# Optimization experiments

Hardware: AMD Instinct MI355X
Metric: run time of the kernel (lower is better)

The kernel has to match this reference:

```python
import jax, jax.numpy as jnp
import numpy as np

B, L, QD, KVD, H = 8, 1024, 1024, 768, 16
DH = QD // H
EPS = 1e-5


def setup_inputs() -> dict:
    key = jax.random.key(0)
    ks = jax.random.split(key, 12)
    q = jax.random.normal(ks[0], (B, L, QD), jnp.float32)
    k = jax.random.normal(ks[1], (B, L, KVD), jnp.float32)
    v = jax.random.normal(ks[2], (B, L, KVD), jnp.float32)
    # key_padding_mask: True = valid token (code masks where ~mask)
    lengths = jax.random.randint(ks[3], (B,), L // 2, L + 1)
    key_padding_mask = jnp.arange(L)[None, :] < lengths[:, None]
    def lin(kk, fan_in, fan_out):
        bound = 1.0 / np.sqrt(fan_in)
        k1, k2 = jax.random.split(kk)
        W = jax.random.uniform(k1, (fan_out, fan_in), jnp.float32, -bound, bound)
        b = jax.random.uniform(k2, (fan_out,), jnp.float32, -bound, bound)
        return W, b
    Wq, bq = lin(ks[4], QD, QD)
    Wk, bk = lin(ks[5], KVD, QD)
    Wv, bv = lin(ks[6], KVD, QD)
    Wo, bo = lin(ks[7], QD, QD)
    gamma = jnp.ones((QD,), jnp.float32)
    beta = jnp.zeros((QD,), jnp.float32)
    return {"q": q, "k": k, "v": v, "key_padding_mask": key_padding_mask,
            "Wq": Wq, "bq": bq, "Wk": Wk, "bk": bk, "Wv": Wv, "bv": bv,
            "Wo": Wo, "bo": bo, "gamma": gamma, "beta": beta}


def reference(q, k, v, key_padding_mask, Wq, bq, Wk, bk, Wv, bv, Wo, bo, gamma, beta):
    Bq, Lq, C = q.shape
    scale = DH ** -0.5
    # projections -> [B, H, L, DH]
    qh = (q @ Wq.T + bq).reshape(Bq, Lq, H, DH).transpose(0, 2, 1, 3)
    kh = (k @ Wk.T + bk).reshape(Bq, Lq, H, DH).transpose(0, 2, 1, 3)
    vh = (v @ Wv.T + bv).reshape(Bq, Lq, H, DH).transpose(0, 2, 1, 3)
    attn = jnp.einsum('bhld,bhmd->bhlm', qh, kh) * scale
    attn = jnp.where(key_padding_mask[:, None, None, :], attn, -jnp.inf)
    p = jax.nn.softmax(attn, axis=-1)
    out = jnp.einsum('bhlm,bhmd->bhld', p, vh).transpose(0, 2, 1, 3).reshape(Bq, Lq, C)
    out = out @ Wo.T + bo  # dropout is identity in eval
    y = out + q
    mu = jnp.mean(y, axis=-1, keepdims=True)
    var = jnp.var(y, axis=-1, keepdims=True)
    return (y - mu) * jax.lax.rsqrt(var + EPS) * gamma + beta
```

## Files before the change

kernel.cpp:

```cpp
#include <hip/hip_runtime.h>
#include <stdint.h>

typedef float f32x4 __attribute__((ext_vector_type(4)));
typedef __bf16 bf16x8 __attribute__((ext_vector_type(8)));
typedef unsigned short u16;

__device__ __forceinline__ void gload_lds16(const void* g, void* l) {
  __builtin_amdgcn_global_load_lds(
      (__attribute__((address_space(1))) void*)(uintptr_t)(g),
      (__attribute__((address_space(3))) void*)(uint32_t)(uintptr_t)(l),
      16, 0, 0);
}

__device__ __forceinline__ u16 f2bf(float x) {
  __bf16 h = (__bf16)x;
  return *(u16*)&h;
}

__global__ __launch_bounds__(256) void cast_all(
    const float* __restrict__ q, const float* __restrict__ k,
    const float* __restrict__ v, const float* __restrict__ wq,
    const float* __restrict__ wk, const float* __restrict__ wv,
    const float* __restrict__ wo, u16* __restrict__ out) {
  const int g = blockIdx.x;
  const float* in;
  int s;
  if (g < 8192) { in = q; s = 0; }
  else if (g < 14336) { in = k; s = 8192; }
  else if (g < 20480) { in = v; s = 14336; }
  else if (g < 21504) { in = wq; s = 20480; }
  else if (g < 22272) { in = wk; s = 21504; }
  else if (g < 23040) { in = wv; s = 22272; }
  else { in = wo; s = 23040; }
  const int li = (g - s) * 256 + threadIdx.x;
  float4 x = *((const float4*)in + li);
  unsigned lo = (unsigned)f2bf(x.x) | ((unsigned)f2bf(x.y) << 16);
  unsigned hi = (unsigned)f2bf(x.z) | ((unsigned)f2bf(x.w) << 16);
  ((uint2*)out)[(size_t)g * 256 + threadIdx.x] = make_uint2(lo, hi);
}

__global__ __launch_bounds__(256) void proj_kernel(
    const u16* __restrict__ qb, const u16* __restrict__ kb,
    const u16* __restrict__ vb, const u16* __restrict__ wqb,
    const u16* __restrict__ wkb, const u16* __restrict__ wvb,
    const float* __restrict__ bq, const float* __restrict__ bk,
    const float* __restrict__ bv, u16* __restrict__ qpb,
    u16* __restrict__ kpb, u16* __restrict__ vtb) {
  __shared__ __align__(16) u16 As[128 * 32];
  __shared__ __align__(16) u16 Bs[128 * 32];
  const int tid = threadIdx.x;
  const int role = blockIdx.y >> 3;
  const int m0 = blockIdx.x * 128, n0 = (blockIdx.y & 7) * 128;
  const int K = (role == 0) ? 1024 : 768;
  const u16* A = (role == 0) ? qb : ((role == 1) ? kb : vb);
  const u16* Bt = (role == 0) ? wqb : ((role == 1) ? wkb : wvb);
  const float* bias = (role == 0) ? bq : ((role == 1) ? bk : bv);
  const int lane = tid & 63, w = tid >> 6;
  const int wr = w >> 1, wc = w & 1;
  const int l16 = lane & 15, lk = lane >> 4;
  const int srow = tid >> 2, schunk = tid & 3;

  const u16* Ap = A + (size_t)(m0 + srow) * K + schunk * 8;
  const u16* Bp = Bt + (size_t)(n0 + srow) * K + schunk * 8;

  f32x4 acc[4][4] = {};

  for (int kt = 0; kt < K; kt += 32) {
#pragma unroll
    for (int p = 0; p < 2; ++p) {
      gload_lds16(Ap + (size_t)p * 64 * K + kt, As + tid * 8 + p * 2048);
      gload_lds16(Bp + (size_t)p * 64 * K + kt, Bs + tid * 8 + p * 2048);
    }
    __syncthreads();
    bf16x8 a[4], b[4];
#pragma unroll
    for (int i = 0; i < 4; ++i)
      a[i] = *(const bf16x8*)(As + (wr * 64 + i * 16 + l16) * 32 + lk * 8);
#pragma unroll
    for (int j = 0; j < 4; ++j)
      b[j] = *(const bf16x8*)(Bs + (wc * 64 + j * 16 + l16) * 32 + lk * 8);
#pragma unroll
    for (int i = 0; i < 4; ++i)
#pragma unroll
      for (int j = 0; j < 4; ++j)
        acc[i][j] = __builtin_amdgcn_mfma_f32_16x16x32_bf16(a[i], b[j], acc[i][j], 0, 0, 0);
    __syncthreads();
  }

#pragma unroll
  for (int i = 0; i < 4; ++i) {
    const int mrow = m0 + wr * 64 + i * 16 + lk * 4;
#pragma unroll
    for (int j = 0; j < 4; ++j) {
      const int col = n0 + wc * 64 + j * 16 + l16;
      const float bval = bias[col];
      if (role == 0) {
#pragma unroll
        for (int r = 0; r < 4; ++r)
          qpb[(size_t)(mrow + r) * 1024 + col] = f2bf(acc[i][j][r] + bval);
      } else if (role == 1) {
#pragma unroll
        for (int r = 0; r < 4; ++r)
          kpb[(size_t)(mrow + r) * 1024 + col] = f2bf(acc[i][j][r] + bval);
      } else {
        const int bb = mrow >> 10, l = mrow & 1023;
        const int hh = col >> 6, dd = col & 63;
        u16 u0 = f2bf(acc[i][j][0] + bval);
        u16 u1 = f2bf(acc[i][j][1] + bval);
        u16 u2 = f2bf(acc[i][j][2] + bval);
        u16 u3 = f2bf(acc[i][j][3] + bval);
        uint2 pkt = make_uint2((unsigned)u0 | ((unsigned)u1 << 16),
                               (unsigned)u2 | ((unsigned)u3 << 16));
        *(uint2*)(vtb + ((size_t)((bb * 16 + hh) * 64 + dd) << 10) + l) = pkt;
      }
    }
  }
}

__global__ __launch_bounds__(256) void attn_kernel(
    const u16* __restrict__ qp, const u16* __restrict__ kp,
    const u16* __restrict__ vt, const int* __restrict__ mask,
    u16* __restrict__ out) {
  __shared__ __align__(16) u16 KV[2][2][64 * 64];
  __shared__ __align__(16) u16 Ps[4][16 * 64];
  const int tid = threadIdx.x;
  const int qt = blockIdx.x, h = blockIdx.y, b = blockIdx.z;
  const int lane = tid & 63, w = tid >> 6;
  const int l16 = lane & 15, lk = lane >> 4;
  const int srow = tid >> 3, schunk = tid & 7;
  const int sw = schunk ^ (srow & 7);

  int cnt = 0;
  {
    const int4* mp = (const int4*)(mask + (b << 10));
#pragma unroll
    for (int i = 0; i < 4; ++i) {
      const int4 mv = mp[lane * 4 + i];
      cnt += (mv.x ? 1 : 0) + (mv.y ? 1 : 0) + (mv.z ? 1 : 0) + (mv.w ? 1 : 0);
    }
#pragma unroll
    for (int off = 1; off < 64; off <<= 1) cnt += __shfl_xor(cnt, off);
  }
  const int ntile = (cnt + 63) >> 6;
  const int rem = cnt & 63;

#pragma unroll
  for (int p = 0; p < 2; ++p) {
    gload_lds16(qp + (((size_t)(b * 1024 + qt * 64 + p * 32 + srow)) << 10) + h * 64 + sw * 8,
                KV[1][0] + tid * 8 + p * 2048);
    gload_lds16(kp + (((size_t)(b * 1024 + p * 32 + srow)) << 10) + h * 64 + sw * 8,
                KV[0][0] + tid * 8 + p * 2048);
    gload_lds16(vt + (((size_t)((b * 16 + h) * 64 + p * 32 + srow)) << 10) + sw * 8,
                KV[0][1] + tid * 8 + p * 2048);
  }
  __syncthreads();
  const int qrow = w * 16 + l16, qs = qrow & 7;
  bf16x8 aq0 = *(const bf16x8*)(KV[1][0] + qrow * 64 + (lk ^ qs) * 8);
  bf16x8 aq1 = *(const bf16x8*)(KV[1][0] + qrow * 64 + ((lk + 4) ^ qs) * 8);
  __syncthreads();

  const float SC2 = 0.18033688011112042f;
  float lsumq = 0.f;
  f32x4 oacc[4] = {};
  const int e7 = l16 & 7;

  int cur = 0;
  for (int kt = 0; kt < ntile; ++kt) {
    if (kt + 1 < ntile) {
#pragma unroll
      for (int p = 0; p < 2; ++p) {
        gload_lds16(kp + (((size_t)(b * 1024 + (kt + 1) * 64 + p * 32 + srow)) << 10) + h * 64 + sw * 8,
                    KV[cur ^ 1][0] + tid * 8 + p * 2048);
        gload_lds16(vt + (((size_t)((b * 16 + h) * 64 + p * 32 + srow)) << 10) + (kt + 1) * 64 + sw * 8,
                    KV[cur ^ 1][1] + tid * 8 + p * 2048);
      }
    }
    const u16* Kb = KV[cur][0];
    const u16* Vb = KV[cur][1];

    f32x4 sfr[4] = {};
    __builtin_amdgcn_s_setprio(1);
#pragma unroll
    for (int nf = 0; nf < 4; ++nf) {
      const int krow = nf * 16 + l16;
      bf16x8 bk0 = *(const bf16x8*)(Kb + krow * 64 + (lk ^ e7) * 8);
      bf16x8 bk1 = *(const bf16x8*)(Kb + krow * 64 + ((lk + 4) ^ e7) * 8);
      sfr[nf] = __builtin_amdgcn_mfma_f32_16x16x32_bf16(bk0, aq0, sfr[nf], 0, 0, 0);
      sfr[nf] = __builtin_amdgcn_mfma_f32_16x16x32_bf16(bk1, aq1, sfr[nf], 0, 0, 0);
    }
    __builtin_amdgcn_s_setprio(0);

    const bool partial = (kt == ntile - 1) && (rem != 0);
    u16* Pw = &Ps[w][0];
#pragma unroll
    for (int nf = 0; nf < 4; ++nf) {
      float pv0 = __builtin_amdgcn_exp2f(sfr[nf][0] * SC2);
      float pv1 = __builtin_amdgcn_exp2f(sfr[nf][1] * SC2);
      float pv2 = __builtin_amdgcn_exp2f(sfr[nf][2] * SC2);
      float pv3 = __builtin_amdgcn_exp2f(sfr[nf][3] * SC2);
      if (partial) {
        const int k0 = nf * 16 + lk * 4;
        pv0 = (k0 + 0 < rem) ? pv0 : 0.f;
        pv1 = (k0 + 1 < rem) ? pv1 : 0.f;
        pv2 = (k0 + 2 < rem) ? pv2 : 0.f;
        pv3 = (k0 + 3 < rem) ? pv3 : 0.f;
      }
      lsumq += (pv0 + pv1) + (pv2 + pv3);
      unsigned lo = (unsigned)f2bf(pv0) | ((unsigned)f2bf(pv1) << 16);
      unsigned hi = (unsigned)f2bf(pv2) | ((unsigned)f2bf(pv3) << 16);
      *(uint2*)(Pw + l16 * 64 + (((nf * 2 + (lk >> 1)) ^ e7) * 8 + (lk & 1) * 4)) =
          make_uint2(lo, hi);
    }

    bf16x8 ap0 = *(const bf16x8*)(Pw + l16 * 64 + ((lk ^ e7) * 8));
    bf16x8 ap1 = *(const bf16x8*)(Pw + l16 * 64 + (((4 + lk) ^ e7) * 8));
    __builtin_amdgcn_s_setprio(1);
#pragma unroll
    for (int nf = 0; nf < 4; ++nf) {
      const int vrow = nf * 16 + l16;
      bf16x8 bv0 = *(const bf16x8*)(Vb + vrow * 64 + (lk ^ e7) * 8);
      bf16x8 bv1 = *(const bf16x8*)(Vb + vrow * 64 + ((lk + 4) ^ e7) * 8);
      oacc[nf] = __builtin_amdgcn_mfma_f32_16x16x32_bf16(ap0, bv0, oacc[nf], 0, 0, 0);
      oacc[nf] = __builtin_amdgcn_mfma_f32_16x16x32_bf16(ap1, bv1, oacc[nf], 0, 0, 0);
    }
    __builtin_amdgcn_s_setprio(0);

    __syncthreads();
    cur ^= 1;
  }

  lsumq += __shfl_xor(lsumq, 16);
  lsumq += __shfl_xor(lsumq, 32);
  float rinv[4];
#pragma unroll
  for (int r = 0; r < 4; ++r) rinv[r] = 1.0f / __shfl(lsumq, lk * 4 + r);

#pragma unroll
  for (int nf = 0; nf < 4; ++nf)
#pragma unroll
    for (int r = 0; r < 4; ++r) {
      const int tok = b * 1024 + qt * 64 + w * 16 + lk * 4 + r;
      const int col = h * 64 + nf * 16 + l16;
      out[((size_t)tok << 10) + col] = f2bf(oacc[nf][r] * rinv[r]);
    }
}

__global__ __launch_bounds__(256) void gemm_o(
    const u16* __restrict__ A, const u16* __restrict__ Bt,
    const float* __restrict__ bias, float* __restrict__ Cf,
    const float* __restrict__ res) {
  __shared__ __align__(16) u16 As[128 * 32];
  __shared__ __align__(16) u16 Bs[128 * 32];
  const int K = 1024, N = 1024;
  const int tid = threadIdx.x;
  const int m0 = blockIdx.x * 128, n0 = blockIdx.y * 128;
  const int lane = tid & 63, w = tid >> 6;
  const int wr = w >> 1, wc = w & 1;
  const int l16 = lane & 15, lk = lane >> 4;
  const int srow = tid >> 2, schunk = tid & 3;

  const u16* Ap = A + (size_t)(m0 + srow) * K + schunk * 8;
  const u16* Bp = Bt + (size_t)(n0 + srow) * K + schunk * 8;

  f32x4 acc[4][4] = {};

  for (int kt = 0; kt < K; kt += 32) {
#pragma unroll
    for (int p = 0; p < 2; ++p) {
      gload_lds16(Ap + (size_t)p * 64 * K + kt, As + tid * 8 + p * 2048);
      gload_lds16(Bp + (size_t)p * 64 * K + kt, Bs + tid * 8 + p * 2048);
    }
    __syncthreads();
    bf16x8 a[4], b[4];
#pragma unroll
    for (int i = 0; i < 4; ++i)
      a[i] = *(const bf16x8*)(As + (wr * 64 + i * 16 + l16) * 32 + lk * 8);
#pragma unroll
    for (int j = 0; j < 4; ++j)
      b[j] = *(const bf16x8*)(Bs + (wc * 64 + j * 16 + l16) * 32 + lk * 8);
#pragma unroll
    for (int i = 0; i < 4; ++i)
#pragma unroll
      for (int j = 0; j < 4; ++j)
        acc[i][j] = __builtin_amdgcn_mfma_f32_16x16x32_bf16(a[i], b[j], acc[i][j], 0, 0, 0);
    __syncthreads();
  }

#pragma unroll
  for (int i = 0; i < 4; ++i) {
    const int mrow = m0 + wr * 64 + i * 16 + lk * 4;
#pragma unroll
    for (int j = 0; j < 4; ++j) {
      const int col = n0 + wc * 64 + j * 16 + l16;
      const float bval = bias[col];
#pragma unroll
      for (int r = 0; r < 4; ++r) {
        const size_t idx = (size_t)(mrow + r) * N + col;
        Cf[idx] = acc[i][j][r] + bval + res[idx];
      }
    }
  }
}

__global__ __launch_bounds__(256) void ln_kernel(float* __restrict__ y,
                                                 const float* __restrict__ gamma,
                                                 const float* __restrict__ beta) {
  __shared__ float ssum[4], ssq[4];
  const int tid = threadIdx.x;
  float* yr = y + ((size_t)blockIdx.x << 10);
  float4 v = *((const float4*)yr + tid);
  float s = v.x + v.y + v.z + v.w;
  float q2 = v.x * v.x + v.y * v.y + v.z * v.z + v.w * v.w;
#pragma unroll
  for (int off = 1; off < 64; off <<= 1) {
    s += __shfl_xor(s, off);
    q2 += __shfl_xor(q2, off);
  }
  if ((tid & 63) == 0) { ssum[tid >> 6] = s; ssq[tid >> 6] = q2; }
  __syncthreads();
  s = ssum[0] + ssum[1] + ssum[2] + ssum[3];
  q2 = ssq[0] + ssq[1] + ssq[2] + ssq[3];
  const float mu = s * (1.0f / 1024.0f);
  const float rstd = rsqrtf(q2 * (1.0f / 1024.0f) - mu * mu + 1e-5f);
  float4 g = *((const float4*)gamma + tid);
  float4 be = *((const float4*)beta + tid);
  float4 o;
  o.x = (v.x - mu) * rstd * g.x + be.x;
  o.y = (v.y - mu) * rstd * g.y + be.y;
  o.z = (v.z - mu) * rstd * g.z + be.z;
  o.w = (v.w - mu) * rstd * g.w + be.w;
  *((float4*)yr + tid) = o;
}

extern "C" void kernel_launch(void* const* d_in, const int* in_sizes, int n_in,
                              void* d_out, int out_size, void* d_ws, size_t ws_size,
                              hipStream_t stream) {
  (void)in_sizes; (void)n_in; (void)out_size; (void)ws_size;
  const float* q = (const float*)d_in[0];
  const float* k = (const float*)d_in[1];
  const float* v = (const float*)d_in[2];
  const int* msk = (const int*)d_in[3];
  const float* Wq = (const float*)d_in[4];
  const float* bq = (const float*)d_in[5];
  const float* Wk = (const float*)d_in[6];
  const float* bk = (const float*)d_in[7];
  const float* Wv = (const float*)d_in[8];
  const float* bv = (const float*)d_in[9];
  const float* Wo = (const float*)d_in[10];
  const float* bo = (const float*)d_in[11];
  const float* gamma = (const float*)d_in[12];
  const float* beta = (const float*)d_in[13];
  float* out = (float*)d_out;

  char* p = (char*)d_ws;
  auto take = [&p](size_t bytes) {
    char* r = p;
    p += (bytes + 255) & ~(size_t)255;
    return r;
  };
  u16* qb = (u16*)take(8192ull * 1024 * 2);
  u16* kb = (u16*)take(8192ull * 768 * 2);
  u16* vb = (u16*)take(8192ull * 768 * 2);
  u16* wqb = (u16*)take(1024ull * 1024 * 2);
  u16* wkb = (u16*)take(1024ull * 768 * 2);
  u16* wvb = (u16*)take(1024ull * 768 * 2);
  u16* wob = (u16*)take(1024ull * 1024 * 2);
  u16* qpb = (u16*)take(8192ull * 1024 * 2);
  u16* kpb = (u16*)take(8192ull * 1024 * 2);
  u16* vtb = (u16*)take(8192ull * 1024 * 2);
  u16* atb = (u16*)take(8192ull * 1024 * 2);

  cast_all<<<dim3(24064), 256, 0, stream>>>(q, k, v, Wq, Wk, Wv, Wo, qb);

  proj_kernel<<<dim3(64, 24), 256, 0, stream>>>(qb, kb, vb, wqb, wkb, wvb,
                                                bq, bk, bv, qpb, kpb, vtb);

  attn_kernel<<<dim3(16, 16, 8), 256, 0, stream>>>(qpb, kpb, vtb, msk, atb);

  gemm_o<<<dim3(64, 8), 256, 0, stream>>>(atb, wob, bo, out, q);

  ln_kernel<<<dim3(8192), 256, 0, stream>>>(out, gamma, beta);
}
```

Baseline: 193.1 us.

## Triple-buffer LDS tiles with async prefetch in projection and output GEMMs

Converts the projection and output-projection GEMM main loops from single-buffered load-sync-compute into a three-stage LDS ring. Tiles are prefetched two iterations ahead with direct global-to-LDS loads, gated by explicit vmcnt waits and raw barriers. MFMA sections are also wrapped in s_setprio. This is meant to hide global memory latency behind matrix math. The cost is triple the LDS footprint, which may lower occupancy, plus hand-managed waitcnt logic that could break if the compiler reorders memory ops.

```diff
diff --git a/kernel.cpp b/kernel.cpp
--- a/kernel.cpp
+++ b/kernel.cpp
@@ -15,6 +15,12 @@
 __device__ __forceinline__ u16 f2bf(float x) {
   __bf16 h = (__bf16)x;
   return *(u16*)&h;
+}
+
+__device__ __forceinline__ void barrier_raw() {
+  __builtin_amdgcn_sched_barrier(0);
+  __builtin_amdgcn_s_barrier();
+  __builtin_amdgcn_sched_barrier(0);
 }
 
 __global__ __launch_bounds__(256) void cast_all(
@@ -46,8 +52,8 @@
     const float* __restrict__ bq, const float* __restrict__ bk,
     const float* __restrict__ bv, u16* __restrict__ qpb,
     u16* __restrict__ kpb, u16* __restrict__ vtb) {
-  __shared__ __align__(16) u16 As[128 * 32];
-  __shared__ __align__(16) u16 Bs[128 * 32];
+  __shared__ __align__(16) u16 As[3][128 * 32];
+  __shared__ __align__(16) u16 Bs[3][128 * 32];
   const int tid = threadIdx.x;
   const int role = blockIdx.y >> 3;
   const int m0 = blockIdx.x * 128, n0 = (blockIdx.y & 7) * 128;
@@ -59,32 +65,55 @@
   const int wr = w >> 1, wc = w & 1;
   const int l16 = lane & 15, lk = lane >> 4;
   const int srow = tid >> 2, schunk = tid & 3;
+  const int nk = K >> 5;
 
   const u16* Ap = A + (size_t)(m0 + srow) * K + schunk * 8;
   const u16* Bp = Bt + (size_t)(n0 + srow) * K + schunk * 8;
 
   f32x4 acc[4][4] = {};
 
-  for (int kt = 0; kt < K; kt += 32) {
+#pragma unroll
+  for (int t = 0; t < 2; ++t)
 #pragma unroll
     for (int p = 0; p < 2; ++p) {
-      gload_lds16(Ap + (size_t)p * 64 * K + kt, As + tid * 8 + p * 2048);
-      gload_lds16(Bp + (size_t)p * 64 * K + kt, Bs + tid * 8 + p * 2048);
-    }
-    __syncthreads();
+      gload_lds16(Ap + (size_t)p * 64 * K + t * 32, As[t] + tid * 8 + p * 2048);
+      gload_lds16(Bp + (size_t)p * 64 * K + t * 32, Bs[t] + tid * 8 + p * 2048);
+    }
+
+  int cur = 0;
+  for (int kt = 0; kt < nk; ++kt) {
+    const int stg = (cur >= 1) ? cur - 1 : 2;
+    if (kt + 2 < nk) {
+      const int ko = (kt + 2) << 5;
+#pragma unroll
+      for (int p = 0; p < 2; ++p) {
+        gload_lds16(Ap + (size_t)p * 64 * K + ko, As[stg] + tid * 8 + p * 2048);
+        gload_lds16(Bp + (size_t)p * 64 * K + ko, Bs[stg] + tid * 8 + p * 2048);
+      }
+      asm volatile("s_waitcnt vmcnt(8)" ::: "memory");
+    } else if (kt + 1 < nk) {
+      asm volatile("s_waitcnt vmcnt(4)" ::: "memory");
+    } else {
+      asm volatile("s_waitcnt vmcnt(0)" ::: "memory");
+    }
+    barrier_raw();
+
     bf16x8 a[4], b[4];
 #pragma unroll
     for (int i = 0; i < 4; ++i)
-      a[i] = *(const bf16x8*)(As + (wr * 64 + i * 16 + l16) * 32 + lk * 8);
+      a[i] = *(const bf16x8*)(As[cur] + (wr * 64 + i * 16 + l16) * 32 + lk * 8);
 #pragma unroll
     for (int j = 0; j < 4; ++j)
-      b[j] = *(const bf16x8*)(Bs + (wc * 64 + j * 16 + l16) * 32 + lk * 8);
+      b[j] = *(const bf16x8*)(Bs[cur] + (wc * 64 + j * 16 + l16) * 32 + lk * 8);
+    __builtin_amdgcn_s_setprio(1);
 #pragma unroll
     for (int i = 0; i < 4; ++i)
 #pragma unroll
       for (int j = 0; j < 4; ++j)
         acc[i][j] = __builtin_amdgcn_mfma_f32_16x16x32_bf16(a[i], b[j], acc[i][j], 0, 0, 0);
-    __syncthreads();
+    __builtin_amdgcn_s_setprio(0);
+    barrier_raw();
+    cur = (cur < 2) ? cur + 1 : 0;
   }
 
 #pragma unroll
@@ -249,9 +278,9 @@
     const u16* __restrict__ A, const u16* __restrict__ Bt,
     const float* __restrict__ bias, float* __restrict__ Cf,
     const float* __restrict__ res) {
-  __shared__ __align__(16) u16 As[128 * 32];
-  __shared__ __align__(16) u16 Bs[128 * 32];
-  const int K = 1024, N = 1024;
+  __shared__ __align__(16) u16 As[3][128 * 32];
+  __shared__ __align__(16) u16 Bs[3][128 * 32];
+  const int K = 1024, N = 1024, nk = 32;
   const int tid = threadIdx.x;
   const int m0 = blockIdx.x * 128, n0 = blockIdx.y * 128;
   const int lane = tid & 63, w = tid >> 6;
@@ -264,26 +293,48 @@
 
   f32x4 acc[4][4] = {};
 
-  for (int kt = 0; kt < K; kt += 32) {
+#pragma unroll
+  for (int t = 0; t < 2; ++t)
 #pragma unroll
     for (int p = 0; p < 2; ++p) {
-      gload_lds16(Ap + (size_t)p * 64 * K + kt, As + tid * 8 + p * 2048);
-      gload_lds16(Bp + (size_t)p * 64 * K + kt, Bs + tid * 8 + p * 2048);
-    }
-    __syncthreads();
+      gload_lds16(Ap + (size_t)p * 64 * K + t * 32, As[t] + tid * 8 + p * 2048);
+      gload_lds16(Bp + (size_t)p * 64 * K + t * 32, Bs[t] + tid * 8 + p * 2048);
+    }
+
+  int cur = 0;
+  for (int kt = 0; kt < nk; ++kt) {
+    const int stg = (cur >= 1) ? cur - 1 : 2;
+    if (kt + 2 < nk) {
+      const int ko = (kt + 2) << 5;
+#pragma unroll
+      for (int p = 0; p < 2; ++p) {
+        gload_lds16(Ap + (size_t)p * 64 * K + ko, As[stg] + tid * 8 + p * 2048);
+        gload_lds16(Bp + (size_t)p * 64 * K + ko, Bs[stg] + tid * 8 + p * 2048);
+      }
+      asm volatile("s_waitcnt vmcnt(8)" ::: "memory");
+    } else if (kt + 1 < nk) {
+      asm volatile("s_waitcnt vmcnt(4)" ::: "memory");
+    } else {
+      asm volatile("s_waitcnt vmcnt(0)" ::: "memory");
+    }
+    barrier_raw();
+
     bf16x8 a[4], b[4];
 #pragma unroll
     for (int i = 0; i < 4; ++i)
-      a[i] = *(const bf16x8*)(As + (wr * 64 + i * 16 + l16) * 32 + lk * 8);
+      a[i] = *(const bf16x8*)(As[cur] + (wr * 64 + i * 16 + l16) * 32 + lk * 8);
 #pragma unroll
     for (int j = 0; j < 4; ++j)
-      b[j] = *(const bf16x8*)(Bs + (wc * 64 + j * 16 + l16) * 32 + lk * 8);
+      b[j] = *(const bf16x8*)(Bs[cur] + (wc * 64 + j * 16 + l16) * 32 + lk * 8);
+    __builtin_amdgcn_s_setprio(1);
 #pragma unroll
     for (int i = 0; i < 4; ++i)
 #pragma unroll
       for (int j = 0; j < 4; ++j)
         acc[i][j] = __builtin_amdgcn_mfma_f32_16x16x32_bf16(a[i], b[j], acc[i][j], 0, 0, 0);
-    __syncthreads();
+    __builtin_amdgcn_s_setprio(0);
+    barrier_raw();
+    cur = (cur < 2) ? cur + 1 : 0;
   }
 
 #pragma unroll
```

Measured after the change: 184.8 us. -4.3%, faster.
